# Optimization experiments

Measured on AMD Instinct MI355X. Metric: run time of the kernel, lower is better.

## Reference

```python
import jax, jax.numpy as jnp
import numpy as np

B, V, C = 2, 6, 96
D, H, W = 48, 48, 48
TH, TW = 96, 96
EPS = 1e-5


def _trilinear_sample_zeros(vol, gx, gy, gz):
    # vol: [B,C,D,H,W]; gx/gy/gz: normalized coords [D,H,W]; align_corners=False, zeros padding
    Dd, Hh, Ww = vol.shape[2], vol.shape[3], vol.shape[4]
    ix = ((gx + 1.0) * Ww - 1.0) * 0.5
    iy = ((gy + 1.0) * Hh - 1.0) * 0.5
    iz = ((gz + 1.0) * Dd - 1.0) * 0.5
    x0 = jnp.floor(ix); y0 = jnp.floor(iy); z0 = jnp.floor(iz)
    tx, ty, tz = ix - x0, iy - y0, iz - z0
    out = jnp.zeros(vol.shape, vol.dtype)
    for dz in (0, 1):
        for dy in (0, 1):
            for dx in (0, 1):
                xc, yc, zc = x0 + dx, y0 + dy, z0 + dz
                w = ((tx if dx else 1.0 - tx) * (ty if dy else 1.0 - ty)
                     * (tz if dz else 1.0 - tz))
                inb = ((xc >= 0) & (xc < Ww) & (yc >= 0) & (yc < Hh)
                       & (zc >= 0) & (zc < Dd))
                xi = jnp.clip(xc, 0, Ww - 1).astype(jnp.int32)
                yi = jnp.clip(yc, 0, Hh - 1).astype(jnp.int32)
                zi = jnp.clip(zc, 0, Dd - 1).astype(jnp.int32)
                val = vol[:, :, zi, yi, xi]  # [B,C,D,H,W]
                out = out + val * (w * inb)[None, None]
    return out


def _resize_bilinear(img, oh, ow):
    # torch F.interpolate(mode='bilinear', align_corners=False) semantics
    h, w = img.shape[-2], img.shape[-1]
    def idx(n_in, n_out):
        scale = n_in / n_out
        src = jnp.maximum(scale * (jnp.arange(n_out) + 0.5) - 0.5, 0.0)
        i0 = jnp.clip(jnp.floor(src).astype(jnp.int32), 0, n_in - 1)
        i1 = jnp.clip(i0 + 1, 0, n_in - 1)
        return i0, i1, (src - i0).astype(img.dtype)
    y0, y1, ty = idx(h, oh)
    x0, x1, tx = idx(w, ow)
    rows = img[..., y0, :] * (1.0 - ty)[:, None] + img[..., y1, :] * ty[:, None]
    return rows[..., x0] * (1.0 - tx) + rows[..., x1] * tx


def _project_one_view(vol, theta):
    # base grid per torch affine_grid(align_corners=False): pixel-center coords in [-1,1]
    zc = (jnp.arange(D) + 0.5) * (2.0 / D) - 1.0
    yc = (jnp.arange(H) + 0.5) * (2.0 / H) - 1.0
    xc = (jnp.arange(W) + 0.5) * (2.0 / W) - 1.0
    Z, Y, X = jnp.meshgrid(zc, yc, xc, indexing='ij')  # [D,H,W]
    c, s = jnp.cos(theta), jnp.sin(theta)
    gx = c * X + s * Z   # rotation about Y axis, rows [c,0,s],[0,1,0],[-s,0,c]
    gy = Y
    gz = -s * X + c * Z
    rotated = _trilinear_sample_zeros(vol, gx, gy, gz)  # [B,C,D,H,W]
    feat2d = rotated.mean(axis=2)                       # depth mean -> [B,C,H,W]
    return _resize_bilinear(feat2d, TH, TW)             # [B,C,TH,TW]


def _post(x, conv1_w, bn_gamma, bn_beta, conv2_w, conv2_b):
    dn = ('NCHW', 'OIHW', 'NCHW')
    x = jax.lax.conv_general_dilated(x, conv1_w, (1, 1), 'SAME', dimension_numbers=dn)
    mu = x.mean(axis=(0, 2, 3), keepdims=True)
    var = ((x - mu) ** 2).mean(axis=(0, 2, 3), keepdims=True)  # biased var, train-mode BN
    x = (x - mu) * jax.lax.rsqrt(var + EPS)
    x = x * bn_gamma[None, :, None, None] + bn_beta[None, :, None, None]
    x = jax.nn.gelu(x, approximate=False)
    x = jax.lax.conv_general_dilated(x, conv2_w, (1, 1), 'SAME', dimension_numbers=dn)
    return x + conv2_b[None, :, None, None]


def setup_inputs() -> dict:
    key = jax.random.key(0)
    k0, k1, k2 = jax.random.split(key, 3)
    voxel_tokens = jax.random.normal(k0, (B, D * H * W, C), jnp.float32)
    view_angles = jnp.linspace(0.0, 2.0 * np.pi, V + 1)[:-1].astype(jnp.float32)
    conv1_w = jax.random.normal(k1, (C, C, 3, 3), jnp.float32) / np.sqrt(C * 9.0)
    bn_gamma = jnp.ones((C,), jnp.float32)
    bn_beta = jnp.zeros((C,), jnp.float32)
    conv2_w = jax.random.normal(k2, (C, C, 1, 1), jnp.float32) / np.sqrt(C)
    conv2_b = jnp.zeros((C,), jnp.float32)
    return dict(voxel_tokens=voxel_tokens, view_angles=view_angles,
                conv1_w=conv1_w, bn_gamma=bn_gamma, bn_beta=bn_beta,
                conv2_w=conv2_w, conv2_b=conv2_b)


def reference(voxel_tokens, view_angles, conv1_w, bn_gamma, bn_beta, conv2_w, conv2_b):
    b = voxel_tokens.shape[0]
    vol = voxel_tokens.transpose(0, 2, 1).reshape(b, C, D, H, W)
    feats = jax.vmap(lambda th: _project_one_view(vol, th))(view_angles)  # [V,B,C,TH,TW]
    # BN stats are computed per-view (torch applies self.post inside the view loop)
    posted = jax.vmap(lambda f: _post(f, conv1_w, bn_gamma, bn_beta, conv2_w, conv2_b))(feats)
    return posted.transpose(1, 0, 2, 3, 4)  # [B,V,C,TH,TW]
```

## Files before the change

kernel.cpp:

```cpp
#include <hip/hip_runtime.h>
#include <math.h>

#define Bn 2
#define Vn 6
#define Cn 96
#define Dn 48
#define Hn 48
#define Wn 48
#define THn 96
#define TWn 96
#define EPSf 1e-5f

#define PD 98
#define NCI8 12

typedef __attribute__((ext_vector_type(8))) short s8v;
typedef __attribute__((ext_vector_type(4))) float f4v;

__device__ __forceinline__ unsigned short f2bf(float f) {
    unsigned int u = __builtin_bit_cast(unsigned int, f);
    u += 0x7FFFu + ((u >> 16) & 1u);
    return (unsigned short)(u >> 16);
}
__device__ __forceinline__ float bf2f(unsigned short h) {
    unsigned int u = ((unsigned int)h) << 16;
    return __builtin_bit_cast(float, u);
}
__device__ __forceinline__ void unpack8(uint4 r, float* f) {
    unsigned int w[4] = {r.x, r.y, r.z, r.w};
#pragma unroll
    for (int j = 0; j < 8; ++j)
        f[j] = bf2f((unsigned short)((w[j >> 1] >> ((j & 1) * 16)) & 0xFFFFu));
}
__device__ __forceinline__ uint4 pack8(const unsigned short* o) {
    uint4 pk;
    pk.x = (unsigned int)o[0] | ((unsigned int)o[1] << 16);
    pk.y = (unsigned int)o[2] | ((unsigned int)o[3] << 16);
    pk.z = (unsigned int)o[4] | ((unsigned int)o[5] << 16);
    pk.w = (unsigned int)o[6] | ((unsigned int)o[7] << 16);
    return pk;
}

__device__ __forceinline__ float gelu_f(float y) {
    float z = y * 0.70710678118654752f;
    float a = fabsf(z);
    float t = __builtin_amdgcn_rcpf(fmaf(0.3275911f, a, 1.0f));
    float e = __builtin_amdgcn_exp2f(-1.4426950408889634f * a * a);
    float p = t * fmaf(t, fmaf(t, fmaf(t, fmaf(t, 1.061405429f,
                                               -1.453152027f),
                                       1.421413741f),
                               -0.284496736f),
                       0.254829592f);
    float er = fmaf(-p, e, 1.0f);
    er = copysignf(er, z);
    return 0.5f * y * (1.0f + er);
}

__global__ __launch_bounds__(256) void k_pre(const float* __restrict__ tokens,
                                             unsigned short* __restrict__ tokB,
                                             const float* __restrict__ w1,
                                             const float* __restrict__ w2,
                                             unsigned short* __restrict__ wAtP,
                                             unsigned short* __restrict__ wCP,
                                             const float* __restrict__ angles,
                                             float4* __restrict__ wtabW,
                                             int4* __restrict__ wtabO) {
    if (blockIdx.x < 10368) {
        int idx = blockIdx.x * 256 + threadIdx.x;
        size_t base = (size_t)idx * 8;
        float4 f0 = *(const float4*)(tokens + base);
        float4 f1 = *(const float4*)(tokens + base + 4);
        unsigned short o[8] = {f2bf(f0.x), f2bf(f0.y), f2bf(f0.z), f2bf(f0.w),
                               f2bf(f1.x), f2bf(f1.y), f2bf(f1.z), f2bf(f1.w)};
        *(uint4*)(&tokB[base]) = pack8(o);
    } else if (blockIdx.x < 10728) {
        int i = (blockIdx.x - 10368) * 256 + threadIdx.x;
        if (i < 82944) {
            int e = i & 7;
            int u = i >> 3;
            int co = u % 96;
            int u2 = u / 96;
            int ci8 = u2 % NCI8;
            int tap = u2 / NCI8;
            wAtP[i] = f2bf(w1[(co * 96 + ci8 * 8 + e) * 9 + tap]);
        } else if (i < 92160) {
            int j = i - 82944;
            int e = j & 7;
            int u = j >> 3;
            int co = u % 96;
            int ci8 = u / 96;
            wCP[j] = f2bf(w2[co * 96 + ci8 * 8 + e]);
        }
    } else {
        int e = (blockIdx.x - 10728) * 256 + threadIdx.x;
        if (e >= 13824) return;
        int z = e % 48;
        int r = e / 48;
        int x = r % 48;
        int v = r / 48;

        float th = angles[v];
        float ct = cosf(th), st = sinf(th);
        float xr = (float)x + 0.5f - 24.0f;
        float zr = (float)z + 0.5f - 24.0f;
        float ix = ct * xr + st * zr + 23.5f;
        float iz = -st * xr + ct * zr + 23.5f;

        float x0f = floorf(ix), z0f = floorf(iz);
        float tx = ix - x0f, tz = iz - z0f;
        int x0 = (int)x0f, z0 = (int)z0f;
        float wx[2] = {1.0f - tx, tx};
        float wz[2] = {1.0f - tz, tz};

        float w[4];
        int o[4];
#pragma unroll
        for (int dz = 0; dz < 2; ++dz) {
            int zc = z0 + dz;
            bool zin = (zc >= 0) && (zc < Dn);
            int zi = min(max(zc, 0), Dn - 1);
#pragma unroll
            for (int dx = 0; dx < 2; ++dx) {
                int xc = x0 + dx;
                bool xin = (xc >= 0) && (xc < Wn);
                int xi = min(max(xc, 0), Wn - 1);
                int k = dz * 2 + dx;
                w[k] = wx[dx] * wz[dz] * ((zin && xin) ? 1.0f : 0.0f) * (1.0f / 48.0f);
                o[k] = (zi * 221184 + xi * 96) * 2;
            }
        }
        wtabW[e] = (float4){w[0], w[1], w[2], w[3]};
        wtabO[e] = (int4){o[0], o[1], o[2], o[3]};
    }
}

__global__ __launch_bounds__(256) void k_feat4(const unsigned short* __restrict__ tokB,
                                               const float4* __restrict__ wtabW,
                                               const int4* __restrict__ wtabO,
                                               unsigned short* __restrict__ featP) {
    int t = threadIdx.x;
    int l = t & 63;
    int h = l >> 5;
    int site = blockIdx.x * 128 + (t >> 6) * 32 + (l & 31);
    int c8 = site % NCI8;
    int r = site / NCI8;
    int x = r % Wn; r /= Wn;
    int y = r % Hn; r /= Hn;
    int b = r & 1;
    int v = r >> 1;
    int vb = v * 2 + b;

    int tb0 = (v * 48 + x) * 48 + h * 24;
    const float4* tw = wtabW + tb0;
    const int4* to = wtabO + tb0;
    const char* tb = (const char*)tokB +
                     ((size_t)b * 10616832 + (size_t)y * 4608 + c8 * 8) * 2;

    float af[8] = {0.f, 0.f, 0.f, 0.f, 0.f, 0.f, 0.f, 0.f};
#pragma unroll 4
    for (int k = 0; k < 24; ++k) {
        float4 w = tw[k];
        int4 o = to[k];
        uint4 r0 = *(const uint4*)(tb + o.x);
        uint4 r1 = *(const uint4*)(tb + o.y);
        uint4 r2 = *(const uint4*)(tb + o.z);
        uint4 r3 = *(const uint4*)(tb + o.w);
        float f0[8], f1[8], f2[8], f3[8];
        unpack8(r0, f0); unpack8(r1, f1); unpack8(r2, f2); unpack8(r3, f3);
#pragma unroll
        for (int j = 0; j < 8; ++j) {
            af[j] += w.x * f0[j] + w.y * f1[j];
            af[j] += w.z * f2[j] + w.w * f3[j];
        }
    }
#pragma unroll
    for (int j = 0; j < 8; ++j) af[j] += __shfl_xor(af[j], 32);

    if (h == 0) {
        unsigned short o[8];
#pragma unroll
        for (int j = 0; j < 8; ++j) o[j] = f2bf(af[j]);
        size_t off = (((size_t)vb * Hn + y) * NCI8 + c8) * Wn + x;
        *(uint4*)(&featP[off * 8]) = pack8(o);
    }
}

__global__ __launch_bounds__(256) void k_resize(const unsigned short* __restrict__ featP,
                                                unsigned short* __restrict__ rz) {
    if (blockIdx.x >= 5184) {
        int hid = (blockIdx.x - 5184) * 256 + threadIdx.x;
        if (hid >= 55872) return;
        int p = hid % 388;
        int r2 = hid / 388;
        int c8 = r2 % NCI8;
        int vb = r2 / NCI8;
        int py, px;
        if (p < 98)      { py = 0;  px = p; }
        else if (p < 196){ py = 97; px = p - 98; }
        else { int q = p - 196; py = 1 + (q >> 1); px = (q & 1) ? 97 : 0; }
        size_t off = (((size_t)vb * PD + py) * NCI8 + c8) * PD + px;
        *(uint4*)(&rz[off * 8]) = (uint4){0u, 0u, 0u, 0u};
        return;
    }
    int idx = blockIdx.x * 256 + threadIdx.x;
    int x = idx % TWn;
    int r = idx / TWn;
    int c8i = r % NCI8; r /= NCI8;
    int y = r % THn;
    int vb = r / THn;

    float sy = fmaxf(0.5f * (y + 0.5f) - 0.5f, 0.0f);
    int y0 = min((int)sy, Hn - 1);
    int y1 = min(y0 + 1, Hn - 1);
    float ty = sy - (float)y0;
    float sx = fmaxf(0.5f * (x + 0.5f) - 0.5f, 0.0f);
    int x0 = min((int)sx, Wn - 1);
    int x1 = min(x0 + 1, Wn - 1);
    float tx = sx - (float)x0;

    const unsigned short* fb = featP + ((size_t)vb * Hn * NCI8 + c8i) * Wn * 8;
    const unsigned short* r0 = fb + (size_t)y0 * (NCI8 * Wn * 8);
    const unsigned short* r1 = fb + (size_t)y1 * (NCI8 * Wn * 8);
    uint4 q00 = *(const uint4*)(r0 + (size_t)x0 * 8);
    uint4 q01 = *(const uint4*)(r0 + (size_t)x1 * 8);
    uint4 q10 = *(const uint4*)(r1 + (size_t)x0 * 8);
    uint4 q11 = *(const uint4*)(r1 + (size_t)x1 * 8);
    float f00[8], f01[8], f10[8], f11[8];
    unpack8(q00, f00); unpack8(q01, f01); unpack8(q10, f10); unpack8(q11, f11);

    float w00 = (1.f - ty) * (1.f - tx), w01 = (1.f - ty) * tx;
    float w10 = ty * (1.f - tx),         w11 = ty * tx;

    unsigned short o[8];
#pragma unroll
    for (int j = 0; j < 8; ++j)
        o[j] = f2bf(w00 * f00[j] + w01 * f01[j] + w10 * f10[j] + w11 * f11[j]);

    size_t off = (((size_t)vb * PD + (y + 1)) * NCI8 + c8i) * PD + (x + 1);
    *(uint4*)(&rz[off * 8]) = pack8(o);
}

__global__ __launch_bounds__(256) void k_conv1(const unsigned short* __restrict__ rz,
                                               const unsigned short* __restrict__ wAtP,
                                               unsigned short* __restrict__ co1) {
    int blk = blockIdx.x;
    int n0 = blk * 128;
    int vb = n0 / 9216;
    int nl0 = n0 - vb * 9216;

    int t = threadIdx.x;
    int wv = t >> 6;
    int l = t & 63;
    int l15 = l & 15, q = l >> 4;

    int nt0 = nl0 + wv * 32;
    int nl[2];
    const unsigned short* pB[2];
#pragma unroll
    for (int i = 0; i < 2; ++i) {
        nl[i] = nt0 + i * 16 + l15;
        int y = nl[i] / 96, x = nl[i] - y * 96;
        pB[i] = rz + ((((size_t)vb * PD + y) * NCI8) * PD + x) * 8;
    }

    f4v acc[2][6];
#pragma unroll
    for (int i = 0; i < 2; ++i)
#pragma unroll
        for (int mt = 0; mt < 6; ++mt) acc[i][mt] = (f4v){0.f, 0.f, 0.f, 0.f};

#pragma unroll
    for (int ks = 0; ks < 3; ++ks) {
        int ci8 = ks * 4 + q;
        const unsigned short* pb0 = pB[0] + (size_t)ci8 * (PD * 8);
        const unsigned short* pb1 = pB[1] + (size_t)ci8 * (PD * 8);
        const unsigned short* pa = wAtP + ((size_t)ci8 * 96 + l15) * 8;
#pragma unroll
        for (int tap = 0; tap < 9; ++tap) {
            int dy = tap / 3, dx = tap % 3;
            size_t toff = ((size_t)dy * (NCI8 * PD) + dx) * 8;
            s8v b0 = *(const s8v*)(pb0 + toff);
            s8v b1 = *(const s8v*)(pb1 + toff);
            const unsigned short* ap = pa + (size_t)tap * (NCI8 * 96 * 8);
#pragma unroll
            for (int mt = 0; mt < 6; ++mt) {
                s8v a = *(const s8v*)(ap + (size_t)mt * (16 * 8));
                acc[0][mt] = __builtin_amdgcn_mfma_f32_16x16x32_bf16(a, b0, acc[0][mt], 0, 0, 0);
                acc[1][mt] = __builtin_amdgcn_mfma_f32_16x16x32_bf16(a, b1, acc[1][mt], 0, 0, 0);
            }
        }
    }

#pragma unroll
    for (int i = 0; i < 2; ++i) {
#pragma unroll
        for (int mt = 0; mt < 6; ++mt) {
            int co0 = mt * 16 + q * 4;
            ushort4 pk;
            pk.x = f2bf(acc[i][mt][0]); pk.y = f2bf(acc[i][mt][1]);
            pk.z = f2bf(acc[i][mt][2]); pk.w = f2bf(acc[i][mt][3]);
            size_t off = (((size_t)vb * NCI8 + (co0 >> 3)) * 9216 + nl[i]) * 8 + (co0 & 7);
            *(ushort4*)(&co1[off]) = pk;
        }
    }
}

__global__ __launch_bounds__(256) void k_stats1(const unsigned short* __restrict__ co1,
                                                float* __restrict__ part) {
    int g = blockIdx.x >> 4;
    int chunk = blockIdx.x & 15;
    int v = g / NCI8;
    int c8 = g % NCI8;
    int t = threadIdx.x;

    float s[8] = {0,0,0,0,0,0,0,0}, ss[8] = {0,0,0,0,0,0,0,0};
    int m0 = chunk * 1152;
    for (int m = m0 + t; m < m0 + 1152; m += 256) {
        int bb = m / 9216;
        int n = m - bb * 9216;
        const unsigned short* p = co1 + (((size_t)(v * 2 + bb) * NCI8 + c8) * 9216 + n) * 8;
        uint4 raw = *(const uint4*)p;
        float f[8];
        unpack8(raw, f);
#pragma unroll
        for (int j = 0; j < 8; ++j) { s[j] += f[j]; ss[j] += f[j] * f[j]; }
    }
#pragma unroll
    for (int off = 1; off < 64; off <<= 1) {
#pragma unroll
        for (int j = 0; j < 8; ++j) {
            s[j]  += __shfl_xor(s[j],  off);
            ss[j] += __shfl_xor(ss[j], off);
        }
    }
    __shared__ float rs[4][8], rss[4][8];
    int wv = t >> 6;
    if ((t & 63) == 0) {
#pragma unroll
        for (int j = 0; j < 8; ++j) { rs[wv][j] = s[j]; rss[wv][j] = ss[j]; }
    }
    __syncthreads();
    if (t < 8) {
        int j = t;
        part[(size_t)blockIdx.x * 16 + j]     = rs[0][j] + rs[1][j] + rs[2][j] + rs[3][j];
        part[(size_t)blockIdx.x * 16 + 8 + j] = rss[0][j] + rss[1][j] + rss[2][j] + rss[3][j];
    }
}

__global__ __launch_bounds__(64) void k_stats2(const float* __restrict__ part,
                                               const float* __restrict__ gamma,
                                               const float* __restrict__ beta,
                                               float* __restrict__ scale,
                                               float* __restrict__ shift) {
    int g = blockIdx.x;
    int t = threadIdx.x;
    int j = t & 7, c = t >> 3;
    size_t b0 = ((size_t)g * 16 + c) * 16;
    size_t b1 = ((size_t)g * 16 + c + 8) * 16;
    float S  = part[b0 + j]     + part[b1 + j];
    float SS = part[b0 + 8 + j] + part[b1 + 8 + j];
#pragma unroll
    for (int off = 8; off < 64; off <<= 1) {
        S  += __shfl_xor(S,  off);
        SS += __shfl_xor(SS, off);
    }
    if (t < 8) {
        int v = g / NCI8, c8 = g % NCI8;
        const float invN = 1.0f / (float)(Bn * THn * TWn);
        float mu = S * invN;
        float var = SS * invN - mu * mu;
        float rstd = rsqrtf(fmaxf(var, 0.0f) + EPSf);
        int ch = c8 * 8 + j;
        float sc = rstd * gamma[ch];
        scale[v * 96 + ch] = sc;
        shift[v * 96 + ch] = beta[ch] - mu * sc;
    }
}

__global__ __launch_bounds__(256) void k_conv2(const unsigned short* __restrict__ co1,
                                               const unsigned short* __restrict__ wCP,
                                               const float* __restrict__ scale,
                                               const float* __restrict__ shift,
                                               const float* __restrict__ b2,
                                               float* __restrict__ out) {
    __shared__ float ssc[96], ssh[96], sbias[96];

    int blk = blockIdx.x;
    int n0 = blk * 64;
    int vb = n0 / 9216;
    int nl0 = n0 - vb * 9216;
    int v = vb >> 1, b = vb & 1;

    int t = threadIdx.x;
    int wv = t >> 6;
    int l = t & 63;
    int l15 = l & 15, q = l >> 4;

    if (t < 96) {
        ssc[t] = scale[v * 96 + t];
        ssh[t] = shift[v * 96 + t];
        sbias[t] = b2[t];
    }
    __syncthreads();

    int n = nl0 + wv * 16 + l15;

    f4v acc[6];
#pragma unroll
    for (int mt = 0; mt < 6; ++mt) acc[mt] = (f4v){0.f, 0.f, 0.f, 0.f};

#pragma unroll
    for (int ks = 0; ks < 3; ++ks) {
        int ci8 = ks * 4 + q;
        int ci0 = ci8 * 8;
        float sc[8], sh[8];
#pragma unroll
        for (int j = 0; j < 8; ++j) { sc[j] = ssc[ci0 + j]; sh[j] = ssh[ci0 + j]; }

        const unsigned short* pb = co1 + (((size_t)vb * NCI8 + ci8) * 9216 + n) * 8;
        uint4 raw = *(const uint4*)pb;
        float f[8];
        unpack8(raw, f);
        unsigned short o[8];
#pragma unroll
        for (int j = 0; j < 8; ++j) {
            float yv = f[j] * sc[j] + sh[j];
            o[j] = f2bf(gelu_f(yv));
        }
        s8v bfr = __builtin_bit_cast(s8v, pack8(o));

        const unsigned short* pa = wCP + ((size_t)ci8 * 96 + l15) * 8;
#pragma unroll
        for (int mt = 0; mt < 6; ++mt) {
            s8v a = *(const s8v*)(pa + (size_t)mt * (16 * 8));
            acc[mt] = __builtin_amdgcn_mfma_f32_16x16x32_bf16(a, bfr, acc[mt], 0, 0, 0);
        }
    }

    size_t obase = ((size_t)(b * Vn + v) * Cn) * 9216;
#pragma unroll
    for (int mt = 0; mt < 6; ++mt) {
        int co0 = mt * 16 + q * 4;
#pragma unroll
        for (int reg = 0; reg < 4; ++reg) {
            int co = co0 + reg;
            out[obase + (size_t)co * 9216 + n] = acc[mt][reg] + sbias[co];
        }
    }
}

extern "C" void kernel_launch(void* const* d_in, const int* in_sizes, int n_in,
                              void* d_out, int out_size, void* d_ws, size_t ws_size,
                              hipStream_t stream) {
    const float* tokens = (const float*)d_in[0];
    const float* angles = (const float*)d_in[1];
    const float* w1     = (const float*)d_in[2];
    const float* gamma  = (const float*)d_in[3];
    const float* beta   = (const float*)d_in[4];
    const float* w2     = (const float*)d_in[5];
    const float* b2     = (const float*)d_in[6];
    float* out = (float*)d_out;

    char* ws = (char*)d_ws;
    unsigned short* featP = (unsigned short*)(ws);
    float* part           = (float*)(ws);
    unsigned short* tokB  = (unsigned short*)(ws + 5308416);
    unsigned short* rz    = (unsigned short*)(ws + 5308416);
    unsigned short* co1   = (unsigned short*)(ws + 27436032);
    float4* wtabW         = (float4*)(ws + 47775744);
    int4*  wtabO          = (int4*)(ws + 47996928);
    unsigned short* wAtP  = (unsigned short*)(ws + 48669696);
    unsigned short* wCP   = (unsigned short*)(ws + 48835584);
    float* scale = (float*)(ws + 48854016);
    float* shift = (float*)(ws + 48856320);

    k_pre<<<10782, 256, 0, stream>>>(tokens, tokB, w1, w2, wAtP, wCP,
                                     angles, wtabW, wtabO);
    k_feat4<<<2592, 256, 0, stream>>>(tokB, wtabW, wtabO, featP);
    k_resize<<<5403, 256, 0, stream>>>(featP, rz);
    k_conv1<<<864, 256, 0, stream>>>(rz, wAtP, co1);
    k_stats1<<<1152, 256, 0, stream>>>(co1, part);
    k_stats2<<<72, 64, 0, stream>>>(part, gamma, beta, scale, shift);
    k_conv2<<<1728, 256, 0, stream>>>(co1, wCP, scale, shift, b2, out);
}
```

Baseline: 286.6 us.

## Split feat and conv1 work across more waves, fold BN finalize into conv2

The projection kernel now splits each site's 48-depth accumulation across four lane groups of 12 steps instead of two groups of 24, doubling the grid and reducing with two xor-shuffles. conv1 splits the 96 output channels across wave pairs (48 each), halving per-wave accumulators and doubling the block count. The tiny stats2 launch is removed and each conv2 block recomputes scale/shift from the partial sums. The aim is more parallelism and latency hiding plus one fewer launch, at the cost of redundant B-fragment loads in conv1 and repeated stats reductions in every conv2 block.

```diff
diff --git a/kernel.cpp b/kernel.cpp
--- a/kernel.cpp
+++ b/kernel.cpp
@@ -134,14 +134,14 @@
     }
 }
 
-__global__ __launch_bounds__(256) void k_feat4(const unsigned short* __restrict__ tokB,
+__global__ __launch_bounds__(256) void k_feat5(const unsigned short* __restrict__ tokB,
                                                const float4* __restrict__ wtabW,
                                                const int4* __restrict__ wtabO,
                                                unsigned short* __restrict__ featP) {
     int t = threadIdx.x;
     int l = t & 63;
-    int h = l >> 5;
-    int site = blockIdx.x * 128 + (t >> 6) * 32 + (l & 31);
+    int h = l >> 4;
+    int site = blockIdx.x * 64 + (t >> 6) * 16 + (l & 15);
     int c8 = site % NCI8;
     int r = site / NCI8;
     int x = r % Wn; r /= Wn;
@@ -150,7 +150,7 @@
     int v = r >> 1;
     int vb = v * 2 + b;
 
-    int tb0 = (v * 48 + x) * 48 + h * 24;
+    int tb0 = (v * 48 + x) * 48 + h * 12;
     const float4* tw = wtabW + tb0;
     const int4* to = wtabO + tb0;
     const char* tb = (const char*)tokB +
@@ -158,7 +158,7 @@
 
     float af[8] = {0.f, 0.f, 0.f, 0.f, 0.f, 0.f, 0.f, 0.f};
 #pragma unroll 4
-    for (int k = 0; k < 24; ++k) {
+    for (int k = 0; k < 12; ++k) {
         float4 w = tw[k];
         int4 o = to[k];
         uint4 r0 = *(const uint4*)(tb + o.x);
@@ -174,7 +174,10 @@
         }
     }
 #pragma unroll
-    for (int j = 0; j < 8; ++j) af[j] += __shfl_xor(af[j], 32);
+    for (int j = 0; j < 8; ++j) {
+        af[j] += __shfl_xor(af[j], 16);
+        af[j] += __shfl_xor(af[j], 32);
+    }
 
     if (h == 0) {
         unsigned short o[8];
@@ -244,16 +247,18 @@
                                                const unsigned short* __restrict__ wAtP,
                                                unsigned short* __restrict__ co1) {
     int blk = blockIdx.x;
-    int n0 = blk * 128;
+    int n0 = blk * 64;
     int vb = n0 / 9216;
     int nl0 = n0 - vb * 9216;
 
     int t = threadIdx.x;
     int wv = t >> 6;
+    int ch = wv & 1;
+    int ns = wv >> 1;
     int l = t & 63;
     int l15 = l & 15, q = l >> 4;
 
-    int nt0 = nl0 + wv * 32;
+    int nt0 = nl0 + ns * 32;
     int nl[2];
     const unsigned short* pB[2];
 #pragma unroll
@@ -263,18 +268,18 @@
         pB[i] = rz + ((((size_t)vb * PD + y) * NCI8) * PD + x) * 8;
     }
 
-    f4v acc[2][6];
+    f4v acc[2][3];
 #pragma unroll
     for (int i = 0; i < 2; ++i)
 #pragma unroll
-        for (int mt = 0; mt < 6; ++mt) acc[i][mt] = (f4v){0.f, 0.f, 0.f, 0.f};
+        for (int mt = 0; mt < 3; ++mt) acc[i][mt] = (f4v){0.f, 0.f, 0.f, 0.f};
 
 #pragma unroll
     for (int ks = 0; ks < 3; ++ks) {
         int ci8 = ks * 4 + q;
         const unsigned short* pb0 = pB[0] + (size_t)ci8 * (PD * 8);
         const unsigned short* pb1 = pB[1] + (size_t)ci8 * (PD * 8);
-        const unsigned short* pa = wAtP + ((size_t)ci8 * 96 + l15) * 8;
+        const unsigned short* pa = wAtP + ((size_t)ci8 * 96 + ch * 48 + l15) * 8;
 #pragma unroll
         for (int tap = 0; tap < 9; ++tap) {
             int dy = tap / 3, dx = tap % 3;
@@ -283,7 +288,7 @@
             s8v b1 = *(const s8v*)(pb1 + toff);
             const unsigned short* ap = pa + (size_t)tap * (NCI8 * 96 * 8);
 #pragma unroll
-            for (int mt = 0; mt < 6; ++mt) {
+            for (int mt = 0; mt < 3; ++mt) {
                 s8v a = *(const s8v*)(ap + (size_t)mt * (16 * 8));
                 acc[0][mt] = __builtin_amdgcn_mfma_f32_16x16x32_bf16(a, b0, acc[0][mt], 0, 0, 0);
                 acc[1][mt] = __builtin_amdgcn_mfma_f32_16x16x32_bf16(a, b1, acc[1][mt], 0, 0, 0);
@@ -294,8 +299,8 @@
 #pragma unroll
     for (int i = 0; i < 2; ++i) {
 #pragma unroll
-        for (int mt = 0; mt < 6; ++mt) {
-            int co0 = mt * 16 + q * 4;
+        for (int mt = 0; mt < 3; ++mt) {
+            int co0 = ch * 48 + mt * 16 + q * 4;
             ushort4 pk;
             pk.x = f2bf(acc[i][mt][0]); pk.y = f2bf(acc[i][mt][1]);
             pk.z = f2bf(acc[i][mt][2]); pk.w = f2bf(acc[i][mt][3]);
@@ -347,40 +352,11 @@
     }
 }
 
-__global__ __launch_bounds__(64) void k_stats2(const float* __restrict__ part,
+__global__ __launch_bounds__(256) void k_conv2(const unsigned short* __restrict__ co1,
+                                               const unsigned short* __restrict__ wCP,
+                                               const float* __restrict__ part,
                                                const float* __restrict__ gamma,
                                                const float* __restrict__ beta,
-                                               float* __restrict__ scale,
-                                               float* __restrict__ shift) {
-    int g = blockIdx.x;
-    int t = threadIdx.x;
-    int j = t & 7, c = t >> 3;
-    size_t b0 = ((size_t)g * 16 + c) * 16;
-    size_t b1 = ((size_t)g * 16 + c + 8) * 16;
-    float S  = part[b0 + j]     + part[b1 + j];
-    float SS = part[b0 + 8 + j] + part[b1 + 8 + j];
-#pragma unroll
-    for (int off = 8; off < 64; off <<= 1) {
-        S  += __shfl_xor(S,  off);
-        SS += __shfl_xor(SS, off);
-    }
-    if (t < 8) {
-        int v = g / NCI8, c8 = g % NCI8;
-        const float invN = 1.0f / (float)(Bn * THn * TWn);
-        float mu = S * invN;
-        float var = SS * invN - mu * mu;
-        float rstd = rsqrtf(fmaxf(var, 0.0f) + EPSf);
-        int ch = c8 * 8 + j;
-        float sc = rstd * gamma[ch];
-        scale[v * 96 + ch] = sc;
-        shift[v * 96 + ch] = beta[ch] - mu * sc;
-    }
-}
-
-__global__ __launch_bounds__(256) void k_conv2(const unsigned short* __restrict__ co1,
-                                               const unsigned short* __restrict__ wCP,
-                                               const float* __restrict__ scale,
-                                               const float* __restrict__ shift,
                                                const float* __restrict__ b2,
                                                float* __restrict__ out) {
     __shared__ float ssc[96], ssh[96], sbias[96];
@@ -397,8 +373,22 @@
     int l15 = l & 15, q = l >> 4;
 
     if (t < 96) {
-        ssc[t] = scale[v * 96 + t];
-        ssh[t] = shift[v * 96 + t];
+        int c8 = t >> 3, j = t & 7;
+        int g = v * NCI8 + c8;
+        float S = 0.f, SS = 0.f;
+#pragma unroll
+        for (int c = 0; c < 16; ++c) {
+            const float* pp = part + ((size_t)g * 16 + c) * 16;
+            S += pp[j];
+            SS += pp[8 + j];
+        }
+        const float invN = 1.0f / (float)(Bn * THn * TWn);
+        float mu = S * invN;
+        float var = SS * invN - mu * mu;
+        float rstd = rsqrtf(fmaxf(var, 0.0f) + EPSf);
+        float sc = rstd * gamma[t];
+        ssc[t] = sc;
+        ssh[t] = beta[t] - mu * sc;
         sbias[t] = b2[t];
     }
     __syncthreads();
@@ -471,15 +461,12 @@
     int4*  wtabO          = (int4*)(ws + 47996928);
     unsigned short* wAtP  = (unsigned short*)(ws + 48669696);
     unsigned short* wCP   = (unsigned short*)(ws + 48835584);
-    float* scale = (float*)(ws + 48854016);
-    float* shift = (float*)(ws + 48856320);
 
     k_pre<<<10782, 256, 0, stream>>>(tokens, tokB, w1, w2, wAtP, wCP,
                                      angles, wtabW, wtabO);
-    k_feat4<<<2592, 256, 0, stream>>>(tokB, wtabW, wtabO, featP);
+    k_feat5<<<5184, 256, 0, stream>>>(tokB, wtabW, wtabO, featP);
     k_resize<<<5403, 256, 0, stream>>>(featP, rz);
-    k_conv1<<<864, 256, 0, stream>>>(rz, wAtP, co1);
+    k_conv1<<<1728, 256, 0, stream>>>(rz, wAtP, co1);
     k_stats1<<<1152, 256, 0, stream>>>(co1, part);
-    k_stats2<<<72, 64, 0, stream>>>(part, gamma, beta, scale, shift);
-    k_conv2<<<1728, 256, 0, stream>>>(co1, wCP, scale, shift, b2, out);
-}
+    k_conv2<<<1728, 256, 0, stream>>>(co1, wCP, part, gamma, beta, b2, out);
+}
```

Result: faster. 270.5 us (-5.6%).
